# Optimization experiments

Hardware: AMD Instinct MI355X
Metric: run time of the kernel (lower is better)

Reference implementation:

```python
import jax, jax.numpy as jnp
import numpy as np


def setup_inputs() -> dict:
    key = jax.random.key(0)
    ks = jax.random.split(key, 5)
    d_out, d_in = 4096, 4096
    r = min(d_out, d_in)
    B, T = 4, 2048
    x = jax.random.normal(ks[0], (B, T, d_in), dtype=jnp.float32)
    U = jax.random.normal(ks[1], (d_out, r), dtype=jnp.float32)
    S = jax.random.uniform(ks[2], (r,), dtype=jnp.float32)
    Vt = jax.random.normal(ks[3], (r, d_in), dtype=jnp.float32)
    epsilon = jnp.zeros((r,), dtype=jnp.float32)
    bias = jax.random.normal(ks[4], (d_out,), dtype=jnp.float32)
    return {"x": x, "U": U, "S": S, "Vt": Vt, "epsilon": epsilon, "bias": bias}


def reference(x, U, S, Vt, epsilon, bias):
    # w = U @ diag(S + epsilon) @ Vt  (diag folded as column scale of U)
    w = (U * (S + epsilon)[None, :]) @ Vt  # [d_out, d_in]
    # F.linear: y = x @ w.T + bias
    return jnp.einsum('btk,ok->bto', x, w) + bias
```

## Files before the change

kernel.cpp:

```cpp
#include <hip/hip_runtime.h>
#include <hip/hip_bf16.h>
#include <stdint.h>

typedef __attribute__((ext_vector_type(4))) float f32x4;
typedef __attribute__((ext_vector_type(8))) short short8v;

typedef __attribute__((address_space(1))) void gvoid;
typedef __attribute__((address_space(3))) void lvoid;

#define GLD16(gp, lp) __builtin_amdgcn_global_load_lds((const gvoid*)(gp), (lvoid*)(lp), 16, 0, 0)

__device__ __forceinline__ unsigned short f2bf(float f) {
    union { float ff; unsigned uu; } a; a.ff = f;
    unsigned u = a.uu;
    u += 0x7FFFu + ((u >> 16) & 1u);
    return (unsigned short)(u >> 16);
}

__global__ __launch_bounds__(256) void prep_u_kernel(
    const float* __restrict__ U, const float* __restrict__ S,
    const float* __restrict__ eps, unsigned short* __restrict__ Ub) {
    long idx = ((long)blockIdx.x * 256 + threadIdx.x) * 8;
    int r = (int)(idx & 4095);
    f32x4 u0 = *(const f32x4*)(U + idx);
    f32x4 u1 = *(const f32x4*)(U + idx + 4);
    f32x4 s0 = *(const f32x4*)(S + r);
    f32x4 s1 = *(const f32x4*)(S + r + 4);
    f32x4 e0 = *(const f32x4*)(eps + r);
    f32x4 e1 = *(const f32x4*)(eps + r + 4);
    union { uint4 v; unsigned short s[8]; } o;
#pragma unroll
    for (int j = 0; j < 4; ++j) {
        o.s[j]     = f2bf(u0[j] * (s0[j] + e0[j]));
        o.s[j + 4] = f2bf(u1[j] * (s1[j] + e1[j]));
    }
    *(uint4*)(Ub + idx) = o.v;
}

__global__ __launch_bounds__(256) void cvt_bf16_kernel(
    const float* __restrict__ src, unsigned short* __restrict__ dst) {
    long idx = ((long)blockIdx.x * 256 + threadIdx.x) * 8;
    f32x4 v0 = *(const f32x4*)(src + idx);
    f32x4 v1 = *(const f32x4*)(src + idx + 4);
    union { uint4 v; unsigned short s[8]; } o;
#pragma unroll
    for (int j = 0; j < 4; ++j) {
        o.s[j]     = f2bf(v0[j]);
        o.s[j + 4] = f2bf(v1[j]);
    }
    *(uint4*)(dst + idx) = o.v;
}

__global__ __launch_bounds__(256) void transpose_cvt_kernel(
    const float* __restrict__ src, unsigned short* __restrict__ dst) {
    __shared__ float tile[64][65];
    int tx = threadIdx.x & 63;
    int tq = threadIdx.x >> 6;
    int r0 = blockIdx.y << 6;
    int k0 = blockIdx.x << 6;
#pragma unroll
    for (int i = 0; i < 16; ++i) {
        int row = (i << 2) + tq;
        tile[row][tx] = src[(long)(r0 + row) * 4096 + k0 + tx];
    }
    __syncthreads();
#pragma unroll
    for (int i = 0; i < 16; ++i) {
        int krow = (i << 2) + tq;
        dst[(long)(k0 + krow) * 4096 + r0 + tx] = f2bf(tile[tx][krow]);
    }
}

#define MM(a, b, c) __builtin_amdgcn_mfma_f32_16x16x32_bf16(a, b, c, 0, 0, 0)

#define ACH(bf, kh) (As + ((bf) * 2 + (kh)) * 8192)
#define BCH(bf, kh) (Bs + ((bf) * 2 + (kh)) * 8192)

#define STAGE_A(bf, kh, koff) do { \
    const unsigned short* _s = A + gAr + (koff); \
    unsigned short* _d = ACH(bf, kh) + wave * 512; \
    GLD16(_s, _d); GLD16(_s + (long)128 * K, _d + 4096); } while (0)

#define STAGE_B(bf, kh, koff) do { \
    const unsigned short* _s = B + gBr + (koff); \
    unsigned short* _d = BCH(bf, kh) + wave * 512; \
    GLD16(_s, _d); GLD16(_s + (long)128 * K, _d + 4096); } while (0)

#define LOAD_A(bf, ks, mh) do { \
    const unsigned short* _p = ACH(bf, ks) + aBase + (mh) * 2048; \
    _Pragma("unroll") \
    for (int _m = 0; _m < 4; ++_m) aR[_m] = *(const short8v*)(_p + _m * 512); } while (0)

#define READ_B(bf, ks) do { \
    const unsigned short* _p = BCH(bf, ks) + bBase; \
    _Pragma("unroll") \
    for (int _n = 0; _n < 4; ++_n) bR[_n] = *(const short8v*)(_p + _n * 512); } while (0)

#define PH_SYNC do { \
    __builtin_amdgcn_s_barrier(); \
    asm volatile("s_waitcnt lgkmcnt(0)" ::: "memory"); } while (0)

#define MFMA16(mh) do { \
    __builtin_amdgcn_s_setprio(1); \
    _Pragma("unroll") \
    for (int _m = 0; _m < 4; ++_m) { \
        acc[(mh) * 4 + _m][0] = MM(aR[_m], bR[0], acc[(mh) * 4 + _m][0]); \
        acc[(mh) * 4 + _m][1] = MM(aR[_m], bR[1], acc[(mh) * 4 + _m][1]); \
        acc[(mh) * 4 + _m][2] = MM(aR[_m], bR[2], acc[(mh) * 4 + _m][2]); \
        acc[(mh) * 4 + _m][3] = MM(aR[_m], bR[3], acc[(mh) * 4 + _m][3]); \
    } \
    __builtin_amdgcn_s_setprio(0); } while (0)

#define VM4 asm volatile("s_waitcnt vmcnt(4)" ::: "memory")
#define PH_END __builtin_amdgcn_s_barrier()

template<int OUT_BF16, int BIAS>
__global__ __launch_bounds__(512, 2) void gemm256_kernel(
    const unsigned short* __restrict__ A,
    const unsigned short* __restrict__ B,
    void* __restrict__ Cv, const float* __restrict__ bias,
    int M, int N, int K) {
    __shared__ unsigned short As[4 * 8192];
    __shared__ unsigned short Bs[4 * 8192];

    const int tid  = threadIdx.x;
    const int wave = tid >> 6;
    const int lane = tid & 63;
    const int fr   = lane & 15;
    const int fq   = lane >> 4;

    const int nwg = gridDim.x;
    const int bid = blockIdx.x;
    const int cpx = nwg >> 3;
    const int wg  = (bid & 7) * cpx + (bid >> 3);
    const int ntn = N >> 8;
    const long m0 = (long)(wg / ntn) << 8;
    const long n0 = (long)(wg % ntn) << 8;

    const int wwr = wave >> 2;
    const int wwc = wave & 3;

    const int  rS  = tid >> 2;
    const int  sS  = (tid & 3) ^ ((rS >> 1) & 3);
    const long gAr = (m0 + rS) * K + sS * 8;
    const long gBr = (n0 + rS) * K + sS * 8;

    const int swz   = (fq ^ ((fr >> 1) & 3)) * 8;
    const int aBase = (wwr * 128 + fr) * 32 + swz;
    const int bBase = (wwc * 64 + fr) * 32 + swz;

    f32x4  acc[8][4] = {};
    short8v aR[4], bR[4];

    STAGE_A(0, 0, 0);  STAGE_B(0, 0, 0);
    STAGE_A(0, 1, 32); STAGE_B(0, 1, 32);
    STAGE_A(1, 0, 64); STAGE_B(1, 0, 64);
    VM4;
    __builtin_amdgcn_s_barrier();

    const int nIter = K >> 7;
    for (int i = 0; i < nIter; ++i) {
        const int kt1off = 128 * i + 96;
        int k3 = 128 * i + 128; if (k3 >= K) k3 -= K;
        int k5 = 128 * i + 160; if (k5 >= K) k5 -= K;
        int k7 = 128 * i + 192; if (k7 >= K) k7 -= K;

        LOAD_A(0, 0, 0); READ_B(0, 0); STAGE_A(1, 1, kt1off);
        PH_SYNC; MFMA16(0); PH_END;
        LOAD_A(0, 0, 1); STAGE_B(1, 1, kt1off);
        PH_SYNC; MFMA16(1); PH_END;
        LOAD_A(0, 1, 0); READ_B(0, 1); STAGE_A(0, 0, k3);
        PH_SYNC; MFMA16(0); PH_END;
        LOAD_A(0, 1, 1); STAGE_B(0, 0, k3);
        PH_SYNC; MFMA16(1); VM4; PH_END;
        LOAD_A(1, 0, 0); READ_B(1, 0); STAGE_A(0, 1, k5);
        PH_SYNC; MFMA16(0); PH_END;
        LOAD_A(1, 0, 1); STAGE_B(0, 1, k5);
        PH_SYNC; MFMA16(1); PH_END;
        LOAD_A(1, 1, 0); READ_B(1, 1); STAGE_A(1, 0, k7);
        PH_SYNC; MFMA16(0); PH_END;
        LOAD_A(1, 1, 1); STAGE_B(1, 0, k7);
        PH_SYNC; MFMA16(1); VM4; PH_END;
    }

#pragma unroll
    for (int nf = 0; nf < 4; ++nf) {
        const int col = (int)n0 + wwc * 64 + nf * 16 + fr;
        float bv = BIAS ? bias[col] : 0.0f;
#pragma unroll
        for (int mf = 0; mf < 8; ++mf) {
            f32x4 v = acc[mf][nf];
            long rowb = m0 + wwr * 128 + mf * 16 + fq * 4;
#pragma unroll
            for (int j = 0; j < 4; ++j) {
                float val = v[j] + bv;
                long off = (rowb + j) * N + col;
                if (OUT_BF16) ((unsigned short*)Cv)[off] = f2bf(val);
                else          ((float*)Cv)[off] = val;
            }
        }
    }
}

extern "C" void kernel_launch(void* const* d_in, const int* in_sizes, int n_in,
                              void* d_out, int out_size, void* d_ws, size_t ws_size,
                              hipStream_t stream) {
    const float* x    = (const float*)d_in[0];
    const float* U    = (const float*)d_in[1];
    const float* S    = (const float*)d_in[2];
    const float* Vt   = (const float*)d_in[3];
    const float* eps  = (const float*)d_in[4];
    const float* bias = (const float*)d_in[5];
    float* out = (float*)d_out;

    char* ws = (char*)d_ws;
    unsigned short* Ub  = (unsigned short*)(ws);
    unsigned short* VtT = (unsigned short*)(ws + (size_t)(32 << 20));
    unsigned short* Wb  = (unsigned short*)(ws + (size_t)(64 << 20));
    unsigned short* Xb  = (unsigned short*)(ws);

    prep_u_kernel<<<8192, 256, 0, stream>>>(U, S, eps, Ub);
    transpose_cvt_kernel<<<dim3(64, 64), 256, 0, stream>>>(Vt, VtT);
    gemm256_kernel<1, 0><<<256, 512, 0, stream>>>(Ub, VtT, (void*)Wb, nullptr,
                                                  4096, 4096, 4096);
    cvt_bf16_kernel<<<16384, 256, 0, stream>>>(x, Xb);
    gemm256_kernel<0, 1><<<512, 512, 0, stream>>>(Xb, Wb, (void*)out, bias,
                                                  8192, 4096, 4096);
}
```

Baseline: 456.8 us.

## Double-buffer LDS-to-register fragments to overlap reads with MFMA

Fragment registers for A and B are now double-buffered, so the LDS reads for the next phase are issued before the MFMA block of the current phase. The explicit lgkmcnt(0) wait before each MFMA phase is removed, which is meant to hide LDS read latency behind matrix math. In exchange, register pressure rises (twice the fragment registers) at launch bounds of 512 threads with 2 blocks, and the barrier/staging order is restructured. Correctness now depends on compiler-inserted waits and on the reordered barriers keeping LDS buffers from being overwritten while still being read.

```diff
diff --git a/kernel.cpp b/kernel.cpp
--- a/kernel.cpp
+++ b/kernel.cpp
@@ -86,33 +86,29 @@
     unsigned short* _d = BCH(bf, kh) + wave * 512; \
     GLD16(_s, _d); GLD16(_s + (long)128 * K, _d + 4096); } while (0)
 
-#define LOAD_A(bf, ks, mh) do { \
+#define LOAD_A_TO(s, bf, ks, mh) do { \
     const unsigned short* _p = ACH(bf, ks) + aBase + (mh) * 2048; \
     _Pragma("unroll") \
-    for (int _m = 0; _m < 4; ++_m) aR[_m] = *(const short8v*)(_p + _m * 512); } while (0)
-
-#define READ_B(bf, ks) do { \
+    for (int _m = 0; _m < 4; ++_m) aR[s][_m] = *(const short8v*)(_p + _m * 512); } while (0)
+
+#define READ_B_TO(s, bf, ks) do { \
     const unsigned short* _p = BCH(bf, ks) + bBase; \
     _Pragma("unroll") \
-    for (int _n = 0; _n < 4; ++_n) bR[_n] = *(const short8v*)(_p + _n * 512); } while (0)
-
-#define PH_SYNC do { \
-    __builtin_amdgcn_s_barrier(); \
-    asm volatile("s_waitcnt lgkmcnt(0)" ::: "memory"); } while (0)
-
-#define MFMA16(mh) do { \
+    for (int _n = 0; _n < 4; ++_n) bR[s][_n] = *(const short8v*)(_p + _n * 512); } while (0)
+
+#define MFMA16S(as, bs, mh) do { \
     __builtin_amdgcn_s_setprio(1); \
     _Pragma("unroll") \
     for (int _m = 0; _m < 4; ++_m) { \
-        acc[(mh) * 4 + _m][0] = MM(aR[_m], bR[0], acc[(mh) * 4 + _m][0]); \
-        acc[(mh) * 4 + _m][1] = MM(aR[_m], bR[1], acc[(mh) * 4 + _m][1]); \
-        acc[(mh) * 4 + _m][2] = MM(aR[_m], bR[2], acc[(mh) * 4 + _m][2]); \
-        acc[(mh) * 4 + _m][3] = MM(aR[_m], bR[3], acc[(mh) * 4 + _m][3]); \
+        acc[(mh) * 4 + _m][0] = MM(aR[as][_m], bR[bs][0], acc[(mh) * 4 + _m][0]); \
+        acc[(mh) * 4 + _m][1] = MM(aR[as][_m], bR[bs][1], acc[(mh) * 4 + _m][1]); \
+        acc[(mh) * 4 + _m][2] = MM(aR[as][_m], bR[bs][2], acc[(mh) * 4 + _m][2]); \
+        acc[(mh) * 4 + _m][3] = MM(aR[as][_m], bR[bs][3], acc[(mh) * 4 + _m][3]); \
     } \
     __builtin_amdgcn_s_setprio(0); } while (0)
 
 #define VM4 asm volatile("s_waitcnt vmcnt(4)" ::: "memory")
-#define PH_END __builtin_amdgcn_s_barrier()
+#define BAR do { __builtin_amdgcn_s_barrier(); asm volatile("" ::: "memory"); } while (0)
 
 template<int OUT_BF16, int BIAS>
 __global__ __launch_bounds__(512, 2) void gemm256_kernel(
@@ -150,13 +146,14 @@
     const int bBase = (wwc * 64 + fr) * 32 + swz;
 
     f32x4  acc[8][4] = {};
-    short8v aR[4], bR[4];
+    short8v aR[2][4], bR[2][4];
 
     STAGE_A(0, 0, 0);  STAGE_B(0, 0, 0);
     STAGE_A(0, 1, 32); STAGE_B(0, 1, 32);
     STAGE_A(1, 0, 64); STAGE_B(1, 0, 64);
     VM4;
-    __builtin_amdgcn_s_barrier();
+    BAR;
+    LOAD_A_TO(1, 0, 0, 0); READ_B_TO(0, 0, 0);
 
     const int nIter = K >> 7;
     for (int i = 0; i < nIter; ++i) {
@@ -165,22 +162,42 @@
         int k5 = 128 * i + 160; if (k5 >= K) k5 -= K;
         int k7 = 128 * i + 192; if (k7 >= K) k7 -= K;
 
-        LOAD_A(0, 0, 0); READ_B(0, 0); STAGE_A(1, 1, kt1off);
-        PH_SYNC; MFMA16(0); PH_END;
-        LOAD_A(0, 0, 1); STAGE_B(1, 1, kt1off);
-        PH_SYNC; MFMA16(1); PH_END;
-        LOAD_A(0, 1, 0); READ_B(0, 1); STAGE_A(0, 0, k3);
-        PH_SYNC; MFMA16(0); PH_END;
-        LOAD_A(0, 1, 1); STAGE_B(0, 0, k3);
-        PH_SYNC; MFMA16(1); VM4; PH_END;
-        LOAD_A(1, 0, 0); READ_B(1, 0); STAGE_A(0, 1, k5);
-        PH_SYNC; MFMA16(0); PH_END;
-        LOAD_A(1, 0, 1); STAGE_B(0, 1, k5);
-        PH_SYNC; MFMA16(1); PH_END;
-        LOAD_A(1, 1, 0); READ_B(1, 1); STAGE_A(1, 0, k7);
-        PH_SYNC; MFMA16(0); PH_END;
-        LOAD_A(1, 1, 1); STAGE_B(1, 0, k7);
-        PH_SYNC; MFMA16(1); VM4; PH_END;
+        STAGE_A(1, 1, kt1off);
+        LOAD_A_TO(0, 0, 0, 1);
+        MFMA16S(1, 0, 0);
+        BAR;
+        STAGE_B(1, 1, kt1off);
+        LOAD_A_TO(1, 0, 1, 0); READ_B_TO(1, 0, 1);
+        MFMA16S(0, 0, 1);
+        BAR;
+        STAGE_A(0, 0, k3);
+        LOAD_A_TO(0, 0, 1, 1);
+        MFMA16S(1, 1, 0);
+        BAR;
+        STAGE_B(0, 0, k3);
+        VM4;
+        BAR;
+        LOAD_A_TO(1, 1, 0, 0); READ_B_TO(0, 1, 0);
+        MFMA16S(0, 1, 1);
+        BAR;
+        STAGE_A(0, 1, k5);
+        LOAD_A_TO(0, 1, 0, 1);
+        MFMA16S(1, 0, 0);
+        BAR;
+        STAGE_B(0, 1, k5);
+        LOAD_A_TO(1, 1, 1, 0); READ_B_TO(1, 1, 1);
+        MFMA16S(0, 0, 1);
+        BAR;
+        STAGE_A(1, 0, k7);
+        LOAD_A_TO(0, 1, 1, 1);
+        MFMA16S(1, 1, 0);
+        BAR;
+        STAGE_B(1, 0, k7);
+        VM4;
+        BAR;
+        LOAD_A_TO(1, 0, 0, 0); READ_B_TO(0, 0, 0);
+        MFMA16S(0, 1, 1);
+        BAR;
     }
 
 #pragma unroll
```

Result: no change. 465.0 us (+1.8%).
